# Performance work log

Measured on AMD Instinct MI355X. Metric: run time of the kernel, lower is better.

The kernel has to match this reference:

```python
import jax, jax.numpy as jnp
import numpy as np

NUM_THING = 80
THING_STUFF_IDS = np.concatenate([np.arange(80), np.arange(80, 133)])  # thing_class_ids + stuff_class_ids
H_OUT, W_OUT = 641, 641
PIXEL_CONF_THR = 0.4
CLASS_CONF_THR = 0.7
NEG = -1e9  # mask value standing in for removing undetected slots


def _resize_bilinear_align_corners(x, h_out, w_out):
    # x: [h_in, w_in, C]; tf.compat.v1.image.resize_bilinear(..., align_corners=True)
    h_in, w_in = x.shape[0], x.shape[1]
    ys = jnp.linspace(0.0, h_in - 1.0, h_out)
    xs = jnp.linspace(0.0, w_in - 1.0, w_out)
    y0 = jnp.floor(ys).astype(jnp.int32)
    x0 = jnp.floor(xs).astype(jnp.int32)
    y1 = jnp.minimum(y0 + 1, h_in - 1)
    x1 = jnp.minimum(x0 + 1, w_in - 1)
    wy = (ys - y0.astype(ys.dtype))[:, None, None]
    wx = (xs - x0.astype(xs.dtype))[None, :, None]
    rows = x[y0] * (1.0 - wy) + x[y1] * wy          # [h_out, w_in, C]
    return rows[:, x0] * (1.0 - wx) + rows[:, x1] * wx  # [h_out, w_out, C]


def setup_inputs() -> dict:
    key = jax.random.key(0)
    k1, k2 = jax.random.split(key)
    pixel_space_mask_logits = jax.random.normal(k1, (161, 161, 128), dtype=jnp.float32)
    transformer_class_probs = jax.random.uniform(k2, (128, 134), dtype=jnp.float32)
    return {"pixel_space_mask_logits": pixel_space_mask_logits,
            "transformer_class_probs": transformer_class_probs}


def reference(pixel_space_mask_logits, transformer_class_probs):
    # --- _get_transformer_class_prediction (void channel dropped first) ---
    probs = transformer_class_probs[:, :-1]                     # [M, C]
    cls_pred = jnp.argmax(probs, axis=-1).astype(jnp.float32)   # [M]
    cls_conf = jnp.max(probs, axis=-1)                          # [M]
    detected = cls_conf >= CLASS_CONF_THR                       # [M] bool
    num_detections = jnp.sum(detected.astype(jnp.int32))
    # index of each detected slot within the detected subset (matches tf.gather order)
    det_subset_index = jnp.cumsum(detected.astype(jnp.int32)) - 1  # [M]

    # --- resize logits to full image (pieces=1 -> single full-width piece) ---
    resized = _resize_bilinear_align_corners(pixel_space_mask_logits, H_OUT, W_OUT)  # [H, W, M]

    # mask out undetected slots instead of gathering (same math, static shape)
    masked = jnp.where(detected[None, None, :], resized, NEG)   # [H, W, M]

    full_max = jnp.max(resized, axis=-1)                        # [H, W]
    det_max = jnp.max(masked, axis=-1)                          # [H, W]
    detected_pixel = (full_max == det_max).astype(jnp.float32)

    pixel_conf = jnp.max(jax.nn.softmax(masked, axis=-1), axis=-1)
    confident_region = (pixel_conf > PIXEL_CONF_THR).astype(jnp.float32) * detected_pixel

    argmax_slot = jnp.argmax(masked, axis=-1)                   # [H, W] slot index
    mask_id_map = det_subset_index[argmax_slot]                 # index within detected subset
    sem_float = cls_pred[argmax_slot]                           # detected_mask_class_pred gathered

    thing_mask = (sem_float < NUM_THING).astype(jnp.float32) * confident_region
    stuff_mask = (sem_float >= NUM_THING).astype(jnp.float32) * confident_region
    semantic_map = jnp.asarray(THING_STUFF_IDS, jnp.int32)[jnp.round(sem_float).astype(jnp.int32)]
    mask_id_map_plus_one = mask_id_map.astype(jnp.int32) + 1

    # --- empty-detection branch (tf.cond) expressed as select ---
    has_det = num_detections > 0
    mask_id_map_plus_one = jnp.where(has_det, mask_id_map_plus_one, jnp.ones_like(mask_id_map_plus_one))
    semantic_map = jnp.where(has_det, semantic_map, jnp.zeros_like(semantic_map))
    thing_mask = jnp.where(has_det, thing_mask, jnp.zeros_like(thing_mask))
    stuff_mask = jnp.where(has_det, stuff_mask, jnp.zeros_like(stuff_mask))
    return (mask_id_map_plus_one, semantic_map, thing_mask, stuff_mask)
```

## Files before the change

kernel.cpp:

```cpp
#include <hip/hip_runtime.h>

#pragma clang fp contract(off)

#define NP 410881

__global__ __launch_bounds__(128) void fused_kernel(
    const float* __restrict__ logits, const float* __restrict__ probs,
    float* __restrict__ out) {
#pragma clang fp contract(off)
  __shared__ float tex[25 * 132];
  __shared__ float s_cls[128];
  __shared__ unsigned long long s_mask[2];
  int tid = threadIdx.x;
  int X0 = blockIdx.x << 4, Y0 = blockIdx.y << 4;

  int strip = tid & 7, py = tid >> 3;
  int cx = strip >> 1, h = strip & 1;
  int cy = py >> 2;
  int xa = X0 + (cx << 2) + (h << 1);
  int y = Y0 + py;

  int tX = blockIdx.x << 2, tY = blockIdx.y << 2;
  float4 stg[7];
#pragma unroll
  for (int k = 0; k < 7; ++k) {
    int f = tid + (k << 7);
    if (f < 800) {
      int r = f / 160;
      int i = f - r * 160;
      int cc = i >> 5, c4 = i & 31;
      int gy = min(tY + r, 160);
      int gx = min(tX + cc, 160);
      stg[k] = *(const float4*)(logits + ((gy * 161 + gx) << 7) + (c4 << 2));
    }
  }

  {
    const float2* row = (const float2*)(probs + tid * 134);
    float mA = -INFINITY, mB = -INFINITY;
    int aA = 0, aB = 1;
#pragma unroll 4
    for (int j = 0; j < 66; ++j) {
      float2 v = row[j];
      if (v.x > mA) { mA = v.x; aA = 2 * j; }
      if (v.y > mB) { mB = v.y; aB = 2 * j + 1; }
    }
    float v132 = probs[tid * 134 + 132];
    if (v132 > mA) { mA = v132; aA = 132; }
    float bv = mA;
    int bi = aA;
    if (mB > bv || (mB == bv && aB < bi)) { bv = mB; bi = aB; }
    s_cls[tid] = (float)bi;
    bool det = bv >= 0.7f;
    unsigned long long b = __ballot(det);
    if ((tid & 63) == 0) s_mask[tid >> 6] = b;
  }

#pragma unroll
  for (int k = 0; k < 7; ++k) {
    int f = tid + (k << 7);
    if (f < 800) {
      int r = f / 160;
      int i = f - r * 160;
      int cc = i >> 5, c4 = i & 31;
      *(float4*)(tex + (r * 5 + cc) * 132 + (c4 << 2)) = stg[k];
    }
  }
  __syncthreads();

  unsigned long long mlo = s_mask[0], mhi = s_mask[1];
  int ndet = __popcll(mlo) + __popcll(mhi);

  if (ndet == 0) {
    if (y < 641) {
      if (xa < 641) {
        int i0 = y * 641 + xa;
        out[i0] = 1.0f; out[NP + i0] = 0.f; out[2 * NP + i0] = 0.f; out[3 * NP + i0] = 0.f;
      }
      if (xa + 1 < 641) {
        int i1 = y * 641 + xa + 1;
        out[i1] = 1.0f; out[NP + i1] = 0.f; out[2 * NP + i1] = 0.f; out[3 * NP + i1] = 0.f;
      }
    }
    return;
  }

  const float* p0 = tex + (cy * 5 + cx) * 132;
  const float* p1 = p0 + 5 * 132;
  float wy = 0.25f * (float)(py & 3);
  float iwy = 1.0f - wy;
  float wx0 = 0.5f * (float)h;
  float wx1 = wx0 + 0.25f;
  float iwx0 = 1.0f - wx0, iwx1 = 1.0f - wx1;

  float m0 = -INFINITY, m1 = -INFINITY;
  int am0 = 0, am1 = 0;
  float T0 = 0.f, T1 = 0.f;
  bool dp0 = true, dp1 = true;

  if (ndet == 128) {
    float ms0[4], ms1[4], Ts0[4], Ts1[4];
    int as0[4], as1[4];
#pragma unroll
    for (int j = 0; j < 4; ++j) {
      ms0[j] = -INFINITY; ms1[j] = -INFINITY;
      Ts0[j] = 0.f; Ts1[j] = 0.f;
      as0[j] = 0; as1[j] = 0;
    }
#define CH(A00, A01, A10, A11, CIDX, J)                                        \
  {                                                                            \
    float r0 = (A00) * iwy + (A10) * wy;                                       \
    float r1 = (A01) * iwy + (A11) * wy;                                       \
    float v0 = r0 * iwx0 + r1 * wx0;                                           \
    float v1 = r0 * iwx1 + r1 * wx1;                                           \
    bool g0 = v0 > ms0[J]; ms0[J] = g0 ? v0 : ms0[J]; as0[J] = g0 ? (CIDX) : as0[J]; \
    bool g1 = v1 > ms1[J]; ms1[J] = g1 ? v1 : ms1[J]; as1[J] = g1 ? (CIDX) : as1[J]; \
    Ts0[J] += __expf(v0);                                                      \
    Ts1[J] += __expf(v1);                                                      \
  }
#pragma unroll 2
    for (int c = 0; c < 128; c += 4) {
      float4 q00 = *(const float4*)(p0 + c);
      float4 q01 = *(const float4*)(p0 + c + 132);
      float4 q10 = *(const float4*)(p1 + c);
      float4 q11 = *(const float4*)(p1 + c + 132);
      CH(q00.x, q01.x, q10.x, q11.x, c + 0, 0);
      CH(q00.y, q01.y, q10.y, q11.y, c + 1, 1);
      CH(q00.z, q01.z, q10.z, q11.z, c + 2, 2);
      CH(q00.w, q01.w, q10.w, q11.w, c + 3, 3);
    }
#undef CH
    m0 = ms0[0]; am0 = as0[0]; m1 = ms1[0]; am1 = as1[0];
#pragma unroll
    for (int j = 1; j < 4; ++j) {
      if (ms0[j] > m0 || (ms0[j] == m0 && as0[j] < am0)) { m0 = ms0[j]; am0 = as0[j]; }
      if (ms1[j] > m1 || (ms1[j] == m1 && as1[j] < am1)) { m1 = ms1[j]; am1 = as1[j]; }
    }
    T0 = (Ts0[0] + Ts0[1]) + (Ts0[2] + Ts0[3]);
    T1 = (Ts1[0] + Ts1[1]) + (Ts1[2] + Ts1[3]);
  } else {
    float rm0 = -INFINITY, rm1 = -INFINITY;
#pragma unroll 4
    for (int c = 0; c < 128; ++c) {
      float a00 = p0[c], a01 = p0[c + 132];
      float a10 = p1[c], a11 = p1[c + 132];
      float r0 = a00 * iwy + a10 * wy;
      float r1 = a01 * iwy + a11 * wy;
      float v0 = r0 * iwx0 + r1 * wx0;
      float v1 = r0 * iwx1 + r1 * wx1;
      rm0 = fmaxf(rm0, v0);
      rm1 = fmaxf(rm1, v1);
      unsigned long long bit = (c < 64) ? (mlo >> c) : (mhi >> (c - 64));
      if (bit & 1) {
        bool g0 = v0 > m0; m0 = g0 ? v0 : m0; am0 = g0 ? c : am0;
        bool g1 = v1 > m1; m1 = g1 ? v1 : m1; am1 = g1 ? c : am1;
        T0 += __expf(v0);
        T1 += __expf(v1);
      }
    }
    dp0 = (rm0 == m0);
    dp1 = (rm1 == m1);
  }

  float cg0 = ((__expf(m0) > 0.4f * T0) && dp0) ? 1.0f : 0.0f;
  float cg1 = ((__expf(m1) > 0.4f * T1) && dp1) ? 1.0f : 0.0f;
  float sem0 = s_cls[am0], sem1 = s_cls[am1];

  float mid0, mid1;
  if (ndet == 128) {
    mid0 = (float)(am0 + 1);
    mid1 = (float)(am1 + 1);
  } else {
    int a = am0;
    unsigned long long ml = (a >= 63) ? mlo : (mlo & ((1ull << (a + 1)) - 1));
    int cnt = __popcll(ml);
    if (a >= 64) {
      unsigned long long mh = (a >= 127) ? mhi : (mhi & ((1ull << (a - 63)) - 1));
      cnt += __popcll(mh);
    }
    mid0 = (float)cnt;
    a = am1;
    ml = (a >= 63) ? mlo : (mlo & ((1ull << (a + 1)) - 1));
    cnt = __popcll(ml);
    if (a >= 64) {
      unsigned long long mh = (a >= 127) ? mhi : (mhi & ((1ull << (a - 63)) - 1));
      cnt += __popcll(mh);
    }
    mid1 = (float)cnt;
  }

  float th0 = (sem0 < 80.f) ? cg0 : 0.f;
  float st0 = cg0 - th0;
  float th1 = (sem1 < 80.f) ? cg1 : 0.f;
  float st1 = cg1 - th1;

  if (y < 641) {
    if (xa < 641) {
      int i0 = y * 641 + xa;
      out[i0] = mid0; out[NP + i0] = sem0; out[2 * NP + i0] = th0; out[3 * NP + i0] = st0;
    }
    if (xa + 1 < 641) {
      int i1 = y * 641 + xa + 1;
      out[i1] = mid1; out[NP + i1] = sem1; out[2 * NP + i1] = th1; out[3 * NP + i1] = st1;
    }
  }
}

extern "C" void kernel_launch(void* const* d_in, const int* in_sizes, int n_in,
                              void* d_out, int out_size, void* d_ws,
                              size_t ws_size, hipStream_t stream) {
  const float* logits = (const float*)d_in[0];
  const float* probs = (const float*)d_in[1];
  float* out = (float*)d_out;
  (void)d_ws; (void)ws_size;

  dim3 grid(41, 41);
  fused_kernel<<<grid, 128, 0, stream>>>(logits, probs, out);
}
```

Before: 102.7 us.

## Split channel reduction across two thread halves and parallelize class argmax with shuffles

Doubles the block to 256 threads. Each half of the block reduces 64 of the 128 mask channels for the same pixels, and the partial max, argmax, exp-sum and raw-max are merged through shared memory after an extra barrier. The per-row class argmax over the probability table is now done cooperatively with 32-lane shuffle reductions instead of one thread scanning a whole row. This raises parallelism and shortens each thread's serial channel loop, at the cost of more shared memory, an additional sync, and half the threads sitting idle during the final output stage.

New measurement: 109.4 us. 1.07x slower.

```diff
diff --git a/kernel.cpp b/kernel.cpp
--- a/kernel.cpp
+++ b/kernel.cpp
@@ -4,27 +4,34 @@
 
 #define NP 410881
 
-__global__ __launch_bounds__(128) void fused_kernel(
+__global__ __launch_bounds__(256) void fused_kernel(
     const float* __restrict__ logits, const float* __restrict__ probs,
     float* __restrict__ out) {
 #pragma clang fp contract(off)
   __shared__ float tex[25 * 132];
   __shared__ float s_cls[128];
-  __shared__ unsigned long long s_mask[2];
+  __shared__ unsigned s_mchunk[4];
+  __shared__ float s_pf[6 * 128];
+  __shared__ int s_pai[2 * 128];
+
   int tid = threadIdx.x;
+  int lane = tid & 63, wv = tid >> 6;
+  int lt = tid & 127;
+  int half = tid >> 7;
+  int cbase = half << 6;
+
   int X0 = blockIdx.x << 4, Y0 = blockIdx.y << 4;
-
-  int strip = tid & 7, py = tid >> 3;
+  int strip = lt & 7, py = lt >> 3;
   int cx = strip >> 1, h = strip & 1;
   int cy = py >> 2;
   int xa = X0 + (cx << 2) + (h << 1);
   int y = Y0 + py;
 
   int tX = blockIdx.x << 2, tY = blockIdx.y << 2;
-  float4 stg[7];
-#pragma unroll
-  for (int k = 0; k < 7; ++k) {
-    int f = tid + (k << 7);
+  float4 stg[4];
+#pragma unroll
+  for (int k = 0; k < 4; ++k) {
+    int f = tid + (k << 8);
     if (f < 800) {
       int r = f / 160;
       int i = f - r * 160;
@@ -36,29 +43,41 @@
   }
 
   {
-    const float2* row = (const float2*)(probs + tid * 134);
-    float mA = -INFINITY, mB = -INFINITY;
-    int aA = 0, aB = 1;
+    unsigned wmask = 0;
+    int hl = lane >> 5;
+    int l5 = lane & 31;
 #pragma unroll 4
-    for (int j = 0; j < 66; ++j) {
-      float2 v = row[j];
-      if (v.x > mA) { mA = v.x; aA = 2 * j; }
-      if (v.y > mB) { mB = v.y; aB = 2 * j + 1; }
-    }
-    float v132 = probs[tid * 134 + 132];
-    if (v132 > mA) { mA = v132; aA = 132; }
-    float bv = mA;
-    int bi = aA;
-    if (mB > bv || (mB == bv && aB < bi)) { bv = mB; bi = aB; }
-    s_cls[tid] = (float)bi;
-    bool det = bv >= 0.7f;
-    unsigned long long b = __ballot(det);
-    if ((tid & 63) == 0) s_mask[tid >> 6] = b;
-  }
-
-#pragma unroll
-  for (int k = 0; k < 7; ++k) {
-    int f = tid + (k << 7);
+    for (int k = 0; k < 16; ++k) {
+      int r = (wv << 5) + (k << 1) + hl;
+      const float2* rp = (const float2*)(probs + r * 134);
+      float2 v1 = rp[2 * l5];
+      float2 v2 = rp[2 * l5 + 1];
+      float2 w = make_float2(-INFINITY, -INFINITY);
+      if (l5 < 3) w = rp[64 + l5];
+      if (l5 == 2) w.y = -INFINITY;
+      float bv = v1.x;
+      int bi = 4 * l5;
+      if (v1.y > bv) { bv = v1.y; bi = 4 * l5 + 1; }
+      if (v2.x > bv) { bv = v2.x; bi = 4 * l5 + 2; }
+      if (v2.y > bv) { bv = v2.y; bi = 4 * l5 + 3; }
+      if (w.x > bv) { bv = w.x; bi = 128 + 2 * l5; }
+      if (w.y > bv) { bv = w.y; bi = 129 + 2 * l5; }
+#pragma unroll
+      for (int off = 1; off <= 16; off <<= 1) {
+        float ov = __shfl_xor(bv, off);
+        int oi = __shfl_xor(bi, off);
+        if (ov > bv || (ov == bv && oi < bi)) { bv = ov; bi = oi; }
+      }
+      if (l5 == 0) s_cls[r] = (float)bi;
+      wmask |= (bv >= 0.7f ? 1u : 0u) << ((k << 1) + hl);
+    }
+    unsigned other = __shfl(wmask, 32);
+    if (lane == 0) s_mchunk[wv] = wmask | other;
+  }
+
+#pragma unroll
+  for (int k = 0; k < 4; ++k) {
+    int f = tid + (k << 8);
     if (f < 800) {
       int r = f / 160;
       int i = f - r * 160;
@@ -68,11 +87,14 @@
   }
   __syncthreads();
 
-  unsigned long long mlo = s_mask[0], mhi = s_mask[1];
+  unsigned long long mlo =
+      s_mchunk[0] | ((unsigned long long)s_mchunk[1] << 32);
+  unsigned long long mhi =
+      s_mchunk[2] | ((unsigned long long)s_mchunk[3] << 32);
   int ndet = __popcll(mlo) + __popcll(mhi);
 
   if (ndet == 0) {
-    if (y < 641) {
+    if (half == 0 && y < 641) {
       if (xa < 641) {
         int i0 = y * 641 + xa;
         out[i0] = 1.0f; out[NP + i0] = 0.f; out[2 * NP + i0] = 0.f; out[3 * NP + i0] = 0.f;
@@ -85,7 +107,7 @@
     return;
   }
 
-  const float* p0 = tex + (cy * 5 + cx) * 132;
+  const float* p0 = tex + (cy * 5 + cx) * 132 + cbase;
   const float* p1 = p0 + 5 * 132;
   float wy = 0.25f * (float)(py & 3);
   float iwy = 1.0f - wy;
@@ -94,9 +116,9 @@
   float iwx0 = 1.0f - wx0, iwx1 = 1.0f - wx1;
 
   float m0 = -INFINITY, m1 = -INFINITY;
-  int am0 = 0, am1 = 0;
+  int am0 = cbase, am1 = cbase;
   float T0 = 0.f, T1 = 0.f;
-  bool dp0 = true, dp1 = true;
+  float rm0 = -INFINITY, rm1 = -INFINITY;
 
   if (ndet == 128) {
     float ms0[4], ms1[4], Ts0[4], Ts1[4];
@@ -105,7 +127,7 @@
     for (int j = 0; j < 4; ++j) {
       ms0[j] = -INFINITY; ms1[j] = -INFINITY;
       Ts0[j] = 0.f; Ts1[j] = 0.f;
-      as0[j] = 0; as1[j] = 0;
+      as0[j] = cbase + j; as1[j] = cbase + j;
     }
 #define CH(A00, A01, A10, A11, CIDX, J)                                        \
   {                                                                            \
@@ -119,15 +141,15 @@
     Ts1[J] += __expf(v1);                                                      \
   }
 #pragma unroll 2
-    for (int c = 0; c < 128; c += 4) {
+    for (int c = 0; c < 64; c += 4) {
       float4 q00 = *(const float4*)(p0 + c);
       float4 q01 = *(const float4*)(p0 + c + 132);
       float4 q10 = *(const float4*)(p1 + c);
       float4 q11 = *(const float4*)(p1 + c + 132);
-      CH(q00.x, q01.x, q10.x, q11.x, c + 0, 0);
-      CH(q00.y, q01.y, q10.y, q11.y, c + 1, 1);
-      CH(q00.z, q01.z, q10.z, q11.z, c + 2, 2);
-      CH(q00.w, q01.w, q10.w, q11.w, c + 3, 3);
+      CH(q00.x, q01.x, q10.x, q11.x, cbase + c + 0, 0);
+      CH(q00.y, q01.y, q10.y, q11.y, cbase + c + 1, 1);
+      CH(q00.z, q01.z, q10.z, q11.z, cbase + c + 2, 2);
+      CH(q00.w, q01.w, q10.w, q11.w, cbase + c + 3, 3);
     }
 #undef CH
     m0 = ms0[0]; am0 = as0[0]; m1 = ms1[0]; am1 = as1[0];
@@ -138,10 +160,11 @@
     }
     T0 = (Ts0[0] + Ts0[1]) + (Ts0[2] + Ts0[3]);
     T1 = (Ts1[0] + Ts1[1]) + (Ts1[2] + Ts1[3]);
+    rm0 = m0; rm1 = m1;
   } else {
-    float rm0 = -INFINITY, rm1 = -INFINITY;
+    unsigned long long mm = half ? mhi : mlo;
 #pragma unroll 4
-    for (int c = 0; c < 128; ++c) {
+    for (int c = 0; c < 64; ++c) {
       float a00 = p0[c], a01 = p0[c + 132];
       float a10 = p1[c], a11 = p1[c + 132];
       float r0 = a00 * iwy + a10 * wy;
@@ -150,17 +173,33 @@
       float v1 = r0 * iwx1 + r1 * wx1;
       rm0 = fmaxf(rm0, v0);
       rm1 = fmaxf(rm1, v1);
-      unsigned long long bit = (c < 64) ? (mlo >> c) : (mhi >> (c - 64));
-      if (bit & 1) {
-        bool g0 = v0 > m0; m0 = g0 ? v0 : m0; am0 = g0 ? c : am0;
-        bool g1 = v1 > m1; m1 = g1 ? v1 : m1; am1 = g1 ? c : am1;
+      if ((mm >> c) & 1) {
+        bool g0 = v0 > m0; m0 = g0 ? v0 : m0; am0 = g0 ? cbase + c : am0;
+        bool g1 = v1 > m1; m1 = g1 ? v1 : m1; am1 = g1 ? cbase + c : am1;
         T0 += __expf(v0);
         T1 += __expf(v1);
       }
     }
-    dp0 = (rm0 == m0);
-    dp1 = (rm1 == m1);
-  }
+  }
+
+  if (half) {
+    s_pf[0 * 128 + lt] = m0; s_pf[1 * 128 + lt] = T0; s_pf[2 * 128 + lt] = rm0;
+    s_pf[3 * 128 + lt] = m1; s_pf[4 * 128 + lt] = T1; s_pf[5 * 128 + lt] = rm1;
+    s_pai[lt] = am0; s_pai[128 + lt] = am1;
+  }
+  __syncthreads();
+  if (half) return;
+
+  {
+    float mh0 = s_pf[0 * 128 + lt], Th0 = s_pf[1 * 128 + lt], rh0 = s_pf[2 * 128 + lt];
+    float mh1 = s_pf[3 * 128 + lt], Th1 = s_pf[4 * 128 + lt], rh1 = s_pf[5 * 128 + lt];
+    int ah0 = s_pai[lt], ah1 = s_pai[128 + lt];
+    if (mh0 > m0) { m0 = mh0; am0 = ah0; }
+    if (mh1 > m1) { m1 = mh1; am1 = ah1; }
+    rm0 = fmaxf(rm0, rh0); rm1 = fmaxf(rm1, rh1);
+    T0 += Th0; T1 += Th1;
+  }
+  bool dp0 = (rm0 == m0), dp1 = (rm1 == m1);
 
   float cg0 = ((__expf(m0) > 0.4f * T0) && dp0) ? 1.0f : 0.0f;
   float cg1 = ((__expf(m1) > 0.4f * T1) && dp1) ? 1.0f : 0.0f;
@@ -215,5 +254,5 @@
   (void)d_ws; (void)ws_size;
 
   dim3 grid(41, 41);
-  fused_kernel<<<grid, 128, 0, stream>>>(logits, probs, out);
+  fused_kernel<<<grid, 256, 0, stream>>>(logits, probs, out);
 }
```
